# Performance work log

Hardware: AMD Instinct MI355X
Metric: run time of the kernel (lower is better)

The kernel has to match this reference:

```python
import jax, jax.numpy as jnp
import numpy as np

THRESHOLD = 0.5
NEG_POS_RATIO = 3
ALPHA = 10.0
N_PRIORS = 8732
N_CLASSES = 21
BATCH = 128
N_OBJ = 32


def cxcy_to_xy(cxcy):
    return jnp.concatenate([cxcy[..., :2] - cxcy[..., 2:] / 2.0,
                            cxcy[..., :2] + cxcy[..., 2:] / 2.0], axis=-1)


def xy_to_cxcy(xy):
    return jnp.concatenate([(xy[..., :2] + xy[..., 2:]) / 2.0,
                            xy[..., 2:] - xy[..., :2]], axis=-1)


def cxcy_to_gcxgcy(cxcy, priors_cxcy):
    return jnp.concatenate([(cxcy[..., :2] - priors_cxcy[..., :2]) / (priors_cxcy[..., 2:] / 10.0),
                            jnp.log(cxcy[..., 2:] / priors_cxcy[..., 2:]) * 5.0], axis=-1)


def find_jaccard_overlap(a, b):
    # a: (M,4) xyxy, b: (P,4) xyxy -> (M,P)
    lt = jnp.maximum(a[:, None, :2], b[None, :, :2])
    rb = jnp.minimum(a[:, None, 2:], b[None, :, 2:])
    wh = jnp.clip(rb - lt, 0.0)
    inter = wh[..., 0] * wh[..., 1]
    area_a = (a[:, 2] - a[:, 0]) * (a[:, 3] - a[:, 1])
    area_b = (b[:, 2] - b[:, 0]) * (b[:, 3] - b[:, 1])
    return inter / (area_a[:, None] + area_b[None, :] - inter)


def _match_one(boxes, labels, priors_xy, priors_cxcy):
    # boxes: (M,4) xyxy, labels: (M,)
    iou = find_jaccard_overlap(boxes, priors_xy)           # (M,P)
    obj_idx = jnp.argmax(iou, axis=1)                      # best prior per object
    iou = iou.at[jnp.arange(boxes.shape[0]), obj_idx].set(1.0)
    positive = (iou >= THRESHOLD).any(axis=0)              # (P,)
    max_prior_idx = jnp.argmax(iou, axis=0)                # best object per prior
    true_cls = labels[max_prior_idx] * positive.astype(labels.dtype)
    matched = boxes[max_prior_idx]                         # (P,4)
    true_locs = cxcy_to_gcxgcy(xy_to_cxcy(matched), priors_cxcy)
    return true_locs, true_cls, positive


def setup_inputs() -> dict:
    key = jax.random.key(0)
    k1, k2, k3, k4, k5, k6 = jax.random.split(key, 6)
    pred_loc = jax.random.normal(k1, (BATCH, N_PRIORS, 4), dtype=jnp.float32)
    pred_cls = jax.random.normal(k2, (BATCH, N_PRIORS, N_CLASSES), dtype=jnp.float32)
    # valid xyxy gt boxes in [0,1]
    p1 = jax.random.uniform(k3, (BATCH, N_OBJ, 2))
    p2 = jax.random.uniform(k4, (BATCH, N_OBJ, 2))
    b_boxes = jnp.concatenate([jnp.minimum(p1, p2), jnp.maximum(p1, p2) + 1e-3], axis=-1)
    b_boxes = jnp.clip(b_boxes, 0.0, 1.0).astype(jnp.float32)
    b_labels = jax.random.randint(k5, (BATCH, N_OBJ), 1, N_CLASSES)
    cxy = jax.random.uniform(k6, (N_PRIORS, 2), minval=0.1, maxval=0.9)
    wh = jax.random.uniform(jax.random.fold_in(k6, 1), (N_PRIORS, 2), minval=0.05, maxval=0.3)
    priors_cxcy = jnp.concatenate([cxy, wh], axis=-1).astype(jnp.float32)
    return {"pred_loc": pred_loc, "pred_cls": pred_cls, "b_boxes": b_boxes,
            "b_labels": b_labels, "priors_cxcy": priors_cxcy}


def reference(pred_loc, pred_cls, b_boxes, b_labels, priors_cxcy):
    batch_size, n_priors, n_classes = pred_cls.shape
    priors_xy = cxcy_to_xy(priors_cxcy)
    true_locs, true_classes, positive = jax.vmap(
        _match_one, in_axes=(0, 0, None, None))(b_boxes, b_labels, priors_xy, priors_cxcy)
    pos_f = positive.astype(pred_loc.dtype)                 # (B,P)
    n_positives = positive.sum(axis=1)                      # (B,)
    n_pos_total = n_positives.sum().astype(pred_loc.dtype)
    # L1 loss (mean over positive box elements)
    loc_loss = (jnp.abs(pred_loc - true_locs) * pos_f[..., None]).sum() / (n_pos_total * 4.0)
    # per-prior cross-entropy
    logp = jax.nn.log_softmax(pred_cls, axis=-1)
    ce = -jnp.take_along_axis(logp, true_classes[..., None], axis=-1)[..., 0]  # (B,P)
    conf_loss_pos = (ce * pos_f).sum()
    # hard negative mining: sort negatives descending per image
    conf_neg = jnp.where(positive, 0.0, ce)
    conf_neg_sorted = -jnp.sort(-conf_neg, axis=1)
    ranks = jnp.arange(n_priors)[None, :]
    hard_mask = ranks < (NEG_POS_RATIO * n_positives)[:, None]
    conf_loss_hard_neg = jnp.where(hard_mask, conf_neg_sorted, 0.0).sum()
    conf_loss = (conf_loss_hard_neg + conf_loss_pos) / n_pos_total
    loc_loss = ALPHA * loc_loss
    total_loss = conf_loss + loc_loss
    return total_loss, loc_loss, conf_loss
```

## Files before the change

### kernel.cpp

```cpp
#include <hip/hip_runtime.h>
#include <math.h>

#define B 128
#define M 32
#define P 8732
#define C 21
#define ALPHA 10.0f
#define TPB2 256
#define PPB 256
#define NB2 35
#define CH 8
#define CS 1092

__global__ __launch_bounds__(256) void k1_partial(
    const float* __restrict__ b_boxes, const float* __restrict__ priors,
    float* __restrict__ pI, float* __restrict__ pU, int* __restrict__ pidx,
    int* __restrict__ done) {
  if (blockIdx.x == 0 && threadIdx.x == 0) *done = 0;
  int b = blockIdx.x >> 3;
  int ch = blockIdx.x & 7;
  int wid = threadIdx.x >> 6;
  int lane = threadIdx.x & 63;
  int obase = wid * 8;

  float ox1[8], oy1[8], ox2[8], oy2[8], oarea[8], bI[8], bU[8];
  int bidx[8];
#pragma unroll
  for (int k = 0; k < 8; k++) {
    float4 bx = ((const float4*)b_boxes)[(size_t)b * M + obase + k];
    ox1[k] = bx.x; oy1[k] = bx.y; ox2[k] = bx.z; oy2[k] = bx.w;
    oarea[k] = (bx.z - bx.x) * (bx.w - bx.y);
    bI[k] = -1.0f; bU[k] = 1.0f; bidx[k] = P;
  }

  int pend = (ch + 1) * CS;
  if (pend > P) pend = P;
#pragma unroll 2
  for (int p = ch * CS + lane; p < pend; p += 64) {
    float4 pr = ((const float4*)priors)[p];
    float pw2 = pr.z * 0.5f, ph2 = pr.w * 0.5f;
    float px1 = pr.x - pw2, py1 = pr.y - ph2;
    float px2 = pr.x + pw2, py2 = pr.y + ph2;
    float areaP = pr.z * pr.w;
#pragma unroll
    for (int k = 0; k < 8; k++) {
      float iw = fminf(ox2[k], px2) - fmaxf(ox1[k], px1);
      float ih = fminf(oy2[k], py2) - fmaxf(oy1[k], py1);
      iw = fmaxf(iw, 0.0f);
      ih = fmaxf(ih, 0.0f);
      float inter = iw * ih;
      float uni = oarea[k] + areaP - inter;
      if (inter * bU[k] > bI[k] * uni) { bI[k] = inter; bU[k] = uni; bidx[k] = p; }
    }
  }
  for (int off = 32; off >= 1; off >>= 1) {
#pragma unroll
    for (int k = 0; k < 8; k++) {
      float oI = __shfl_xor(bI[k], off, 64);
      float oU = __shfl_xor(bU[k], off, 64);
      int oi = __shfl_xor(bidx[k], off, 64);
      float l = oI * bU[k], r = bI[k] * oU;
      if (l > r || (l == r && oi < bidx[k])) { bI[k] = oI; bU[k] = oU; bidx[k] = oi; }
    }
  }
  if (lane == 0) {
#pragma unroll
    for (int k = 0; k < 8; k++) {
      int idx = ((size_t)b * M + obase + k) * CH + ch;
      pI[idx] = bI[k]; pU[idx] = bU[k]; pidx[idx] = bidx[k];
    }
  }
}

__global__ __launch_bounds__(TPB2) void k2_perprior(
    const float* __restrict__ pred_loc, const float* __restrict__ pred_cls,
    const float* __restrict__ b_boxes, const int* __restrict__ b_labels,
    const float* __restrict__ priors,
    const float* __restrict__ pI, const float* __restrict__ pU,
    const int* __restrict__ pidx,
    float* __restrict__ ploc, float* __restrict__ pce, int* __restrict__ pnp,
    float* __restrict__ confneg) {
  int b = blockIdx.y;
  int p0 = blockIdx.x * PPB;
  int tid = threadIdx.x;
  int wid = tid >> 6;
  int lane = tid & 63;

  __shared__ __align__(16) float sCls[4 * 64 * C];
  __shared__ float sx1[M], sy1[M], sx2[M], sy2[M], sarea[M];
  __shared__ int slab[M], sobj[M];
  __shared__ int sinv[PPB];

  sinv[tid] = 0x7fffffff;
  if (tid < M) {
    int m = tid;
    float4 bx = ((const float4*)b_boxes)[b * M + m];
    sx1[m] = bx.x; sy1[m] = bx.y; sx2[m] = bx.z; sy2[m] = bx.w;
    sarea[m] = (bx.z - bx.x) * (bx.w - bx.y);
    slab[m] = b_labels[b * M + m];
    int o = b * M + m;
    float cI = pI[o * CH], cU = pU[o * CH];
    int ci = pidx[o * CH];
#pragma unroll
    for (int ch = 1; ch < CH; ch++) {
      float nI = pI[o * CH + ch], nU = pU[o * CH + ch];
      int ni = pidx[o * CH + ch];
      if (nI * cU > cI * nU) { cI = nI; cU = nU; ci = ni; }
    }
    sobj[m] = ci;
  }
  __syncthreads();
  if (tid < M) {
    int t = sobj[tid] - p0;
    if (t >= 0 && t < PPB) atomicMin(&sinv[t], tid);
  }
  {
    int wp0 = p0 + wid * 64;
    int nv = P - wp0;
    nv = nv < 0 ? 0 : (nv > 64 ? 64 : nv);
    int nf4 = (nv * C) >> 2;
    const float4* src = (const float4*)(pred_cls + ((size_t)b * P + wp0) * C);
    float4* dst = (float4*)&sCls[wid * 64 * C];
    for (int i = lane; i < nf4; i += 64) dst[i] = src[i];
  }
  __syncthreads();

  float locpart = 0.0f, cepospart = 0.0f;
  int npos = 0;
  int p = p0 + tid;
  if (p < P) {
    float4 pr = ((const float4*)priors)[p];
    float pw2 = pr.z * 0.5f, ph2 = pr.w * 0.5f;
    float px1 = pr.x - pw2, py1 = pr.y - ph2;
    float px2 = pr.x + pw2, py2 = pr.y + ph2;
    float areaP = pr.z * pr.w;
    float bI = -1.0f, bU = 1.0f;
    int bm = 0;
    for (int m = 0; m < M; m++) {
      float iw = fminf(sx2[m], px2) - fmaxf(sx1[m], px1);
      float ih = fminf(sy2[m], py2) - fmaxf(sy1[m], py1);
      iw = fmaxf(iw, 0.0f);
      ih = fmaxf(ih, 0.0f);
      float inter = iw * ih;
      float uni = sarea[m] + areaP - inter;
      if (inter * bU > bI * uni) { bI = inter; bU = uni; bm = m; }
    }
    int fm = sinv[tid];
    if (fm != 0x7fffffff) {
      if (!((bI == bU) && (bm < fm))) { bI = 1.0f; bU = 1.0f; bm = fm; }
    }
    bool pos = (2.0f * bI >= bU);
    int wAny = __any((int)pos);

    if (wAny) {
      float4 pl = ((const float4*)pred_loc)[(size_t)b * P + p];
      float bx1 = sx1[bm], by1 = sy1[bm], bx2 = sx2[bm], by2 = sy2[bm];
      float cx = (bx1 + bx2) * 0.5f, cy = (by1 + by2) * 0.5f;
      float w = bx2 - bx1, h = by2 - by1;
      float rz = __builtin_amdgcn_rcpf(pr.z);
      float rw = __builtin_amdgcn_rcpf(pr.w);
      float g0 = (cx - pr.x) * 10.0f * rz;
      float g1 = (cy - pr.y) * 10.0f * rw;
      float g2 = __logf(w * rz) * 5.0f;
      float g3 = __logf(h * rw) * 5.0f;
      if (pos) {
        locpart = fabsf(pl.x - g0) + fabsf(pl.y - g1) +
                  fabsf(pl.z - g2) + fabsf(pl.w - g3);
        npos = 1;
      }
    }

    const float* u = &sCls[(wid * 64 + lane) * C];
    int cls = pos ? slab[bm] : 0;
    float se = 0.0f, vc = 0.0f;
#pragma unroll
    for (int c = 0; c < C; c++) {
      float x = u[c];
      se += __expf(x);
      if (c == cls) vc = x;
    }
    float lse = __logf(se);
    float ce = lse - vc;
    confneg[(size_t)b * P + p] = pos ? 0.0f : ce;
    cepospart = pos ? ce : 0.0f;
  }

  for (int off = 32; off >= 1; off >>= 1) {
    locpart += __shfl_down(locpart, off, 64);
    cepospart += __shfl_down(cepospart, off, 64);
    npos += __shfl_down(npos, off, 64);
  }
  __shared__ float rloc[4], rce[4];
  __shared__ int rnp[4];
  if (lane == 0) { rloc[wid] = locpart; rce[wid] = cepospart; rnp[wid] = npos; }
  __syncthreads();
  if (tid == 0) {
    int f = b * NB2 + blockIdx.x;
    ploc[f] = rloc[0] + rloc[1] + rloc[2] + rloc[3];
    pce[f] = rce[0] + rce[1] + rce[2] + rce[3];
    pnp[f] = rnp[0] + rnp[1] + rnp[2] + rnp[3];
  }
}

__global__ __launch_bounds__(1024) void k3_hardneg(
    const float* __restrict__ confneg,
    const float* __restrict__ ploc, const float* __restrict__ pce,
    const int* __restrict__ pnp,
    float* __restrict__ imgres, int* __restrict__ done,
    float* __restrict__ out) {
  int b = blockIdx.x;
  int tid = threadIdx.x;
  int wid = tid >> 6;
  int lane = tid & 63;

  __shared__ __align__(16) float s[P];
  __shared__ int histw[16 * 256];
  __shared__ __align__(16) int cnt[256];
  __shared__ int sdig, scum, sK, sLast;
  __shared__ float sLoc, sCe, sNp;
  __shared__ float rsum[16], rl[16], rc[16], rh[16], rn[16];
  __shared__ int rcnt[16];

  {
    const float4* row4 = (const float4*)(confneg + (size_t)b * P);
    for (int i = tid; i < P / 4; i += 1024) ((float4*)s)[i] = row4[i];
  }

  if (wid == 0) {
    float lp = 0.0f, cp = 0.0f;
    int np = 0;
    if (lane < NB2) {
      int f = b * NB2 + lane;
      lp = ploc[f]; cp = pce[f]; np = pnp[f];
    }
    for (int off = 32; off >= 1; off >>= 1) {
      lp += __shfl_down(lp, off, 64);
      cp += __shfl_down(cp, off, 64);
      np += __shfl_down(np, off, 64);
    }
    if (lane == 0) {
      int K = np * 3;
      if (K > P) K = P;
      sK = K; sLoc = lp; sCe = cp; sNp = (float)np;
    }
  }
  __syncthreads();

  int K = sK;
  unsigned pfx = 0;
  int Krem = K;
#pragma unroll
  for (int pass = 3; pass >= 0; --pass) {
    int sh = pass * 8;
    for (int i = tid; i < 16 * 256; i += 1024) histw[i] = 0;
    __syncthreads();
    unsigned himask = (pass == 3) ? 0u : (0xFFFFFFFFu << (sh + 8));
    int* myh = &histw[wid * 256];
    for (int i = tid; i < P; i += 1024) {
      unsigned ub = __float_as_uint(s[i]);
      if ((ub & himask) == pfx) atomicAdd(&myh[(ub >> sh) & 255], 1);
    }
    __syncthreads();
    if (tid < 256) {
      int c = 0;
#pragma unroll
      for (int w = 0; w < 16; w++) c += histw[w * 256 + tid];
      cnt[tid] = c;
    }
    __syncthreads();
    if (wid == 0) {
      int4 c4 = ((const int4*)cnt)[lane];
      int s3 = c4.w;
      int s2 = c4.z + s3;
      int s1 = c4.y + s2;
      int s0 = c4.x + s1;
      int suf = s0;
      for (int off = 1; off < 64; off <<= 1) {
        int t = __shfl_down(suf, off, 64);
        if (lane + off < 64) suf += t;
      }
      int above = suf - s0;
      int S0 = above + s0, S1 = above + s1, S2 = above + s2, S3 = above + s3;
      int S4 = above;
      if (S3 >= Krem && S4 < Krem) { sdig = 4 * lane + 3; scum = S4; }
      else if (S2 >= Krem && S3 < Krem) { sdig = 4 * lane + 2; scum = S3; }
      else if (S1 >= Krem && S2 < Krem) { sdig = 4 * lane + 1; scum = S2; }
      else if (S0 >= Krem && S1 < Krem) { sdig = 4 * lane + 0; scum = S1; }
    }
    __syncthreads();
    pfx |= ((unsigned)sdig) << sh;
    Krem -= scum;
  }
  float tau = __uint_as_float(pfx);

  float sum = 0.0f;
  int cgt = 0;
  for (int i = tid; i < P; i += 1024) {
    float v = s[i];
    if (v > tau) { sum += v; cgt++; }
  }
  for (int off = 32; off >= 1; off >>= 1) {
    sum += __shfl_down(sum, off, 64);
    cgt += __shfl_down(cgt, off, 64);
  }
  if (lane == 0) { rsum[wid] = sum; rcnt[wid] = cgt; }
  __syncthreads();
  if (tid == 0) {
    float stot = 0.0f;
    int ctot = 0;
#pragma unroll
    for (int w = 0; w < 16; w++) { stot += rsum[w]; ctot += rcnt[w]; }
    float hard = stot + (float)(K - ctot) * tau;
    imgres[b * 4 + 0] = sLoc;
    imgres[b * 4 + 1] = sCe;
    imgres[b * 4 + 2] = hard;
    imgres[b * 4 + 3] = sNp;
    __threadfence();
    int prev = atomicAdd(done, 1);
    sLast = (prev == B - 1) ? 1 : 0;
  }
  __syncthreads();
  if (sLast) {
    __threadfence();
    float l = 0.0f, c = 0.0f, h = 0.0f, n = 0.0f;
    if (tid < B) {
      l = atomicAdd(&imgres[tid * 4 + 0], 0.0f);
      c = atomicAdd(&imgres[tid * 4 + 1], 0.0f);
      h = atomicAdd(&imgres[tid * 4 + 2], 0.0f);
      n = atomicAdd(&imgres[tid * 4 + 3], 0.0f);
    }
    for (int off = 32; off >= 1; off >>= 1) {
      l += __shfl_down(l, off, 64);
      c += __shfl_down(c, off, 64);
      h += __shfl_down(h, off, 64);
      n += __shfl_down(n, off, 64);
    }
    if (lane == 0) { rl[wid] = l; rc[wid] = c; rh[wid] = h; rn[wid] = n; }
    __syncthreads();
    if (tid == 0) {
      float L = 0, Cc = 0, H = 0, N = 0;
#pragma unroll
      for (int w = 0; w < 16; w++) { L += rl[w]; Cc += rc[w]; H += rh[w]; N += rn[w]; }
      float loc = ALPHA * L / (N * 4.0f);
      float conf = (H + Cc) / N;
      out[0] = conf + loc;
      out[1] = loc;
      out[2] = conf;
    }
  }
}

extern "C" void kernel_launch(void* const* d_in, const int* in_sizes, int n_in,
                              void* d_out, int out_size, void* d_ws, size_t ws_size,
                              hipStream_t stream) {
  (void)in_sizes; (void)n_in; (void)out_size; (void)ws_size;
  const float* pred_loc = (const float*)d_in[0];
  const float* pred_cls = (const float*)d_in[1];
  const float* b_boxes = (const float*)d_in[2];
  const int* b_labels = (const int*)d_in[3];
  const float* priors = (const float*)d_in[4];
  float* out = (float*)d_out;

  int* done = (int*)d_ws;
  float* ploc = (float*)d_ws + 8;
  float* pce = ploc + B * NB2;
  int* pnp = (int*)(pce + B * NB2);
  float* imgres = (float*)(pnp + B * NB2);
  float* pI = imgres + B * 4;
  float* pU = pI + B * M * CH;
  int* pidx = (int*)(pU + B * M * CH);
  float* confneg = (float*)(pidx + B * M * CH);

  k1_partial<<<B * CH, 256, 0, stream>>>(b_boxes, priors, pI, pU, pidx, done);
  dim3 g2(NB2, B);
  k2_perprior<<<g2, TPB2, 0, stream>>>(pred_loc, pred_cls, b_boxes, b_labels,
                                       priors, pI, pU, pidx,
                                       ploc, pce, pnp, confneg);
  k3_hardneg<<<B, 1024, 0, stream>>>(confneg, ploc, pce, pnp, imgres, done, out);
}
```

Measured before the change: 221.6 us.

## Process two 64-prior tiles per wave with register-prefetched class logits

Each block now covers 512 priors instead of 256. Each wave handles two 64-prior tiles in sequence. The wave loads the next tile's pred_cls logits and prior box into registers while it computes IoU matching and cross-entropy for the current tile, so the global load overlaps the compute. Per-wave staging in shared memory replaces the block-wide copy, and the box coordinates move to a float4 shared array. In exchange there are half as many blocks (fewer waves in flight) and more register use from the six prefetch float4s.

```diff
diff --git a/kernel.cpp b/kernel.cpp
--- a/kernel.cpp
+++ b/kernel.cpp
@@ -6,9 +6,9 @@
 #define P 8732
 #define C 21
 #define ALPHA 10.0f
-#define TPB2 256
-#define PPB 256
-#define NB2 35
+#define TILE 64
+#define PPB 512
+#define NB2 18
 #define CH 8
 #define CS 1092
 
@@ -72,7 +72,7 @@
   }
 }
 
-__global__ __launch_bounds__(TPB2) void k2_perprior(
+__global__ __launch_bounds__(256) void k2_perprior(
     const float* __restrict__ pred_loc, const float* __restrict__ pred_cls,
     const float* __restrict__ b_boxes, const int* __restrict__ b_labels,
     const float* __restrict__ priors,
@@ -86,16 +86,18 @@
   int wid = tid >> 6;
   int lane = tid & 63;
 
-  __shared__ __align__(16) float sCls[4 * 64 * C];
-  __shared__ float sx1[M], sy1[M], sx2[M], sy2[M], sarea[M];
+  __shared__ __align__(16) float sCls[4][TILE * C];
+  __shared__ __align__(16) float4 sbox[M];
+  __shared__ float sarea[M];
   __shared__ int slab[M], sobj[M];
   __shared__ int sinv[PPB];
 
   sinv[tid] = 0x7fffffff;
+  sinv[tid + 256] = 0x7fffffff;
   if (tid < M) {
     int m = tid;
     float4 bx = ((const float4*)b_boxes)[b * M + m];
-    sx1[m] = bx.x; sy1[m] = bx.y; sx2[m] = bx.z; sy2[m] = bx.w;
+    sbox[m] = bx;
     sarea[m] = (bx.z - bx.x) * (bx.w - bx.y);
     slab[m] = b_labels[b * M + m];
     int o = b * M + m;
@@ -114,63 +116,108 @@
     int t = sobj[tid] - p0;
     if (t >= 0 && t < PPB) atomicMin(&sinv[t], tid);
   }
-  {
-    int wp0 = p0 + wid * 64;
-    int nv = P - wp0;
-    nv = nv < 0 ? 0 : (nv > 64 ? 64 : nv);
-    int nf4 = (nv * C) >> 2;
-    const float4* src = (const float4*)(pred_cls + ((size_t)b * P + wp0) * C);
-    float4* dst = (float4*)&sCls[wid * 64 * C];
-    for (int i = lane; i < nf4; i += 64) dst[i] = src[i];
-  }
   __syncthreads();
 
   float locpart = 0.0f, cepospart = 0.0f;
   int npos = 0;
-  int p = p0 + tid;
-  if (p < P) {
-    float4 pr = ((const float4*)priors)[p];
-    float pw2 = pr.z * 0.5f, ph2 = pr.w * 0.5f;
-    float px1 = pr.x - pw2, py1 = pr.y - ph2;
-    float px2 = pr.x + pw2, py2 = pr.y + ph2;
-    float areaP = pr.z * pr.w;
+
+  int tp0 = p0 + (wid * 2) * TILE;
+  int tp1 = tp0 + TILE;
+
+  float4 q[6];
+  float4 prv;
+  {
+    int nv = P - tp0;
+    nv = nv < 0 ? 0 : (nv > TILE ? TILE : nv);
+    if (nv > 0) {
+      int nf4 = (nv * C) >> 2;
+      const float4* src = (const float4*)(pred_cls + ((size_t)b * P + tp0) * C);
+#pragma unroll
+      for (int k = 0; k < 6; k++) {
+        int idx = lane + (k << 6);
+        q[k] = src[idx < nf4 ? idx : 0];
+      }
+      prv = ((const float4*)priors)[tp0 + (lane < nv ? lane : 0)];
+    }
+  }
+
+#pragma unroll
+  for (int t = 0; t < 2; t++) {
+    int ctp = (t == 0) ? tp0 : tp1;
+    int nv = P - ctp;
+    nv = nv < 0 ? 0 : (nv > TILE ? TILE : nv);
+    if (nv == 0) break;
+    int nf4 = (nv * C) >> 2;
+
+    {
+      float4* dst = (float4*)&sCls[wid][0];
+#pragma unroll
+      for (int k = 0; k < 6; k++) {
+        int idx = lane + (k << 6);
+        if (idx < nf4) dst[idx] = q[k];
+      }
+    }
+    float4 myPr = prv;
+
+    if (t == 0) {
+      int nnv = P - tp1;
+      nnv = nnv < 0 ? 0 : (nnv > TILE ? TILE : nnv);
+      if (nnv > 0) {
+        int nnf4 = (nnv * C) >> 2;
+        const float4* src = (const float4*)(pred_cls + ((size_t)b * P + tp1) * C);
+#pragma unroll
+        for (int k = 0; k < 6; k++) {
+          int idx = lane + (k << 6);
+          q[k] = src[idx < nnf4 ? idx : 0];
+        }
+        prv = ((const float4*)priors)[tp1 + (lane < nnv ? lane : 0)];
+      }
+    }
+
+    bool act = lane < nv;
+    int p = ctp + (act ? lane : 0);
+    float pw2 = myPr.z * 0.5f, ph2 = myPr.w * 0.5f;
+    float px1 = myPr.x - pw2, py1 = myPr.y - ph2;
+    float px2 = myPr.x + pw2, py2 = myPr.y + ph2;
+    float areaP = myPr.z * myPr.w;
     float bI = -1.0f, bU = 1.0f;
     int bm = 0;
     for (int m = 0; m < M; m++) {
-      float iw = fminf(sx2[m], px2) - fmaxf(sx1[m], px1);
-      float ih = fminf(sy2[m], py2) - fmaxf(sy1[m], py1);
+      float4 bx = sbox[m];
+      float iw = fminf(bx.z, px2) - fmaxf(bx.x, px1);
+      float ih = fminf(bx.w, py2) - fmaxf(bx.y, py1);
       iw = fmaxf(iw, 0.0f);
       ih = fmaxf(ih, 0.0f);
       float inter = iw * ih;
       float uni = sarea[m] + areaP - inter;
       if (inter * bU > bI * uni) { bI = inter; bU = uni; bm = m; }
     }
-    int fm = sinv[tid];
+    int fm = sinv[ctp - p0 + lane];
     if (fm != 0x7fffffff) {
       if (!((bI == bU) && (bm < fm))) { bI = 1.0f; bU = 1.0f; bm = fm; }
     }
-    bool pos = (2.0f * bI >= bU);
+    bool pos = act && (2.0f * bI >= bU);
     int wAny = __any((int)pos);
 
     if (wAny) {
       float4 pl = ((const float4*)pred_loc)[(size_t)b * P + p];
-      float bx1 = sx1[bm], by1 = sy1[bm], bx2 = sx2[bm], by2 = sy2[bm];
-      float cx = (bx1 + bx2) * 0.5f, cy = (by1 + by2) * 0.5f;
-      float w = bx2 - bx1, h = by2 - by1;
-      float rz = __builtin_amdgcn_rcpf(pr.z);
-      float rw = __builtin_amdgcn_rcpf(pr.w);
-      float g0 = (cx - pr.x) * 10.0f * rz;
-      float g1 = (cy - pr.y) * 10.0f * rw;
+      float4 bx = sbox[bm];
+      float cx = (bx.x + bx.z) * 0.5f, cy = (bx.y + bx.w) * 0.5f;
+      float w = bx.z - bx.x, h = bx.w - bx.y;
+      float rz = __builtin_amdgcn_rcpf(myPr.z);
+      float rw = __builtin_amdgcn_rcpf(myPr.w);
+      float g0 = (cx - myPr.x) * 10.0f * rz;
+      float g1 = (cy - myPr.y) * 10.0f * rw;
       float g2 = __logf(w * rz) * 5.0f;
       float g3 = __logf(h * rw) * 5.0f;
       if (pos) {
-        locpart = fabsf(pl.x - g0) + fabsf(pl.y - g1) +
-                  fabsf(pl.z - g2) + fabsf(pl.w - g3);
-        npos = 1;
+        locpart += fabsf(pl.x - g0) + fabsf(pl.y - g1) +
+                   fabsf(pl.z - g2) + fabsf(pl.w - g3);
+        npos++;
       }
     }
 
-    const float* u = &sCls[(wid * 64 + lane) * C];
+    const float* u = &sCls[wid][lane * C];
     int cls = pos ? slab[bm] : 0;
     float se = 0.0f, vc = 0.0f;
 #pragma unroll
@@ -179,10 +226,11 @@
       se += __expf(x);
       if (c == cls) vc = x;
     }
-    float lse = __logf(se);
-    float ce = lse - vc;
-    confneg[(size_t)b * P + p] = pos ? 0.0f : ce;
-    cepospart = pos ? ce : 0.0f;
+    float ce = __logf(se) - vc;
+    if (act) {
+      confneg[(size_t)b * P + p] = pos ? 0.0f : ce;
+      cepospart += pos ? ce : 0.0f;
+    }
   }
 
   for (int off = 32; off >= 1; off >>= 1) {
@@ -373,8 +421,8 @@
 
   k1_partial<<<B * CH, 256, 0, stream>>>(b_boxes, priors, pI, pU, pidx, done);
   dim3 g2(NB2, B);
-  k2_perprior<<<g2, TPB2, 0, stream>>>(pred_loc, pred_cls, b_boxes, b_labels,
-                                       priors, pI, pU, pidx,
-                                       ploc, pce, pnp, confneg);
+  k2_perprior<<<g2, 256, 0, stream>>>(pred_loc, pred_cls, b_boxes, b_labels,
+                                      priors, pI, pU, pidx,
+                                      ploc, pce, pnp, confneg);
   k3_hardneg<<<B, 1024, 0, stream>>>(confneg, ploc, pce, pnp, imgres, done, out);
 }
```

Result: slower. 241.4 us (+8.9%).
